# Kernel optimization log

Measured on AMD Instinct MI355X. Metric: run time of the kernel, lower is better.

The kernel has to match this reference:

```python
import jax, jax.numpy as jnp
import numpy as np

EPS = 1e-8  # torch.cosine_similarity default eps


def _gelu(x):
    # torch nn.GELU default = exact (erf) gelu
    return jax.nn.gelu(x, approximate=False)


def setup_inputs() -> dict:
    key = jax.random.key(0)
    ks = jax.random.split(key, 12)
    B, D, H1, E, N, K = 32768, 768, 256, 128, 500, 5
    TOT = D + E + 1 + 1 + 4  # 902, importance_net input dim
    s = 0.02
    return {
        "cue": jax.random.normal(ks[0], (B, D), jnp.float32),
        "internal_state": jnp.zeros((B, E), jnp.float32),
        "reward": jax.random.uniform(ks[1], (B, 1), dtype=jnp.float32),
        "timestamp": jax.random.uniform(ks[2], (B, 1), dtype=jnp.float32),
        "emotional_state": jax.random.uniform(ks[3], (B, 4), dtype=jnp.float32),
        "centroids": jax.random.normal(ks[4], (N, E), jnp.float32),
        "enc_w1": jax.random.normal(ks[5], (D, H1), jnp.float32) * s,
        "enc_b1": jnp.zeros((H1,), jnp.float32),
        "enc_w2": jax.random.normal(ks[6], (H1, E), jnp.float32) * s,
        "enc_b2": jnp.zeros((E,), jnp.float32),
        "imp_w1": jax.random.normal(ks[7], (TOT, 64), jnp.float32) * s,
        "imp_b1": jnp.zeros((64,), jnp.float32),
        "imp_w2": jax.random.normal(ks[8], (64, 1), jnp.float32) * s,
        "imp_b2": jnp.zeros((1,), jnp.float32),
        "top_k": K,
    }


def reference(cue, internal_state, reward, timestamp, emotional_state, centroids,
              enc_w1, enc_b1, enc_w2, enc_b2,
              imp_w1, imp_b1, imp_w2, imp_b2, top_k):
    # --- encoder MLP (batched over all cues instead of per-item calls) ---
    enc = _gelu(cue @ enc_w1 + enc_b1) @ enc_w2 + enc_b2        # [B, 128]

    # --- cosine similarity vs all cluster centroids (fused loop) ---
    num = enc @ centroids.T                                      # [B, N]
    e_n = jnp.linalg.norm(enc, axis=-1, keepdims=True)           # [B, 1]
    c_n = jnp.linalg.norm(centroids, axis=-1)                    # [N]
    sims = num / jnp.maximum(e_n * c_n[None, :], EPS)            # [B, N]
    top_vals, _ = jax.lax.top_k(sims, top_k)                     # [B, K]

    # --- importance net on combined memory entry ---
    combined = jnp.concatenate(
        [cue, internal_state, reward, timestamp, emotional_state], axis=-1)  # [B, 902]
    imp = jax.nn.sigmoid(_gelu(combined @ imp_w1 + imp_b1) @ imp_w2 + imp_b2)  # [B, 1]
    imp = imp * jnp.mean(emotional_state, axis=-1, keepdims=True)

    return jnp.concatenate([top_vals, imp], axis=-1)             # [B, K+1]
```

## Files before the change

kernel.cpp:

```cpp
#include <hip/hip_runtime.h>
#include <hip/hip_bf16.h>
#include <hip/hip_fp16.h>
#include <math.h>

using f32x4  = __attribute__((ext_vector_type(4))) float;
using half8  = __attribute__((ext_vector_type(8))) _Float16;
using uint4v = __attribute__((ext_vector_type(4))) unsigned int;

#define WAITV(N) asm volatile("s_waitcnt vmcnt(" #N ")" ::: "memory")
#define LGKM0    asm volatile("s_waitcnt lgkmcnt(0)" ::: "memory")

__device__ __forceinline__ unsigned short f32_to_f16u(float f) {
  return __half_as_ushort(__float2half(f));
}
__device__ __forceinline__ float f16u_to_f32(unsigned short h) {
  return __half2float(__ushort_as_half(h));
}
__device__ __forceinline__ unsigned int pk2(float a, float b) {
  return (unsigned int)f32_to_f16u(a) | ((unsigned int)f32_to_f16u(b) << 16);
}
__device__ __forceinline__ f32x4 mfma16(half8 a, half8 b, f32x4 c) {
  return __builtin_amdgcn_mfma_f32_16x16x32_f16(a, b, c, 0, 0, 0);
}
__device__ __forceinline__ void gload_lds16(void* lds, const void* g) {
  __builtin_amdgcn_global_load_lds(
      (const __attribute__((address_space(1))) unsigned int*)g,
      (__attribute__((address_space(3))) unsigned int*)lds, 16, 0, 0);
}
__device__ __forceinline__ float gelu_exact(float x) {
  return 0.5f * x * (1.0f + erff(x * 0.70710678118654752440f));
}


__global__ __launch_bounds__(256) void k_prep(
    const float* __restrict__ enc_w1, const float* __restrict__ enc_w2,
    const float* __restrict__ imp_w1, const float* __restrict__ cent,
    const float* __restrict__ reward, const float* __restrict__ tsp,
    const float* __restrict__ emo,
    unsigned short* __restrict__ W1T, unsigned short* __restrict__ W2T,
    unsigned short* __restrict__ impW1T, unsigned short* __restrict__ centC,
    float* __restrict__ c_n, unsigned short* __restrict__ tail) {
  int idx = blockIdx.x * 256 + threadIdx.x;
  if (idx < 256 * 768) {
    int n = idx / 768, k = idx - n * 768;
    W1T[idx] = f32_to_f16u(enc_w1[k * 256 + n]);
  }
  if (idx < 128 * 256) {
    int n = idx >> 8, k = idx & 255;
    W2T[idx] = f32_to_f16u(enc_w2[k * 128 + n]);
  }
  if (idx < 64 * 960) {
    int n = idx / 960, k = idx - n * 960;
    impW1T[idx] = (k < 902) ? f32_to_f16u(imp_w1[k * 64 + n]) : (unsigned short)0;
  }
  if (idx < 512 * 128) {
    int n = idx >> 7, k = idx & 127;
    centC[idx] = (n < 500) ? f32_to_f16u(cent[n * 128 + k]) : (unsigned short)0;
  }
  if (idx < 512) {
    float s = 0.f;
    if (idx < 500) {
      const f32x4* p = (const f32x4*)(cent + idx * 128);
#pragma unroll 8
      for (int j = 0; j < 32; ++j) {
        f32x4 v = p[j];
#pragma unroll
        for (int e = 0; e < 4; ++e) {
          float q = (float)(_Float16)v[e];
          s += q * q;
        }
      }
    }
    c_n[idx] = sqrtf(s);
  }
  if (idx < 32768) {
    f32x4 e4 = *(const f32x4*)(emo + (size_t)idx * 4);
    unsigned short* tp = tail + (size_t)idx * 8;
    tp[0] = f32_to_f16u(reward[idx]);
    tp[1] = f32_to_f16u(tsp[idx]);
    tp[2] = f32_to_f16u(e4[0]); tp[3] = f32_to_f16u(e4[1]);
    tp[4] = f32_to_f16u(e4[2]); tp[5] = f32_to_f16u(e4[3]);
    tp[6] = 0; tp[7] = 0;
  }
}

__global__ __launch_bounds__(512, 4) void k_encimp(
    const float* __restrict__ cue, const float* __restrict__ internal,
    const float* __restrict__ emo,
    const unsigned short* __restrict__ W1T, const unsigned short* __restrict__ impW1T,
    const unsigned short* __restrict__ tail,
    const float* __restrict__ b1, const float* __restrict__ ib1,
    const float* __restrict__ iw2, const float* __restrict__ ib2,
    unsigned short* __restrict__ h1, float* __restrict__ out) {
  __shared__ unsigned char sm[73728];
  const int t = threadIdx.x;
  const int lane = t & 63, w = t >> 6;
  const int wr = w >> 2, wc = w & 3;
  const int g = lane >> 4, c = lane & 15;
  const int row0 = blockIdx.x * 64;

  const int srow = t >> 3, q8 = t & 7;
  const int abyte = srow * 128 + q8 * 16;
  const int aswz = (srow & 7) << 4;
  const int myrow = row0 + srow;

  f32x4 aLo, aHi;
  auto issueA = [&](int j) {
    const float* s = (j < 12)
        ? (cue + (size_t)myrow * 768 + j * 64 + q8 * 8)
        : (internal + (size_t)myrow * 128 + (j - 12) * 64 + q8 * 8);
    aLo = *(const f32x4*)s;
    aHi = *(const f32x4*)(s + 4);
  };
  auto convWrite = [&](int buf) {
    uint4v u = {pk2(aLo[0], aLo[1]), pk2(aLo[2], aLo[3]),
                pk2(aHi[0], aHi[1]), pk2(aHi[2], aHi[3])};
    *(uint4v*)(sm + buf * 8192 + (abyte ^ aswz)) = u;
  };
  auto issueB1 = [&](int j) {
#pragma unroll
    for (int i = 0; i < 4; ++i) {
      int L = i * 8192 + t * 16;
      int nl = L >> 7, x = L & 127;
      gload_lds16(sm + 24576 + i * 8192 + w * 1024,
                  (const unsigned char*)W1T + ((size_t)nl * 768 + j * 64) * 2 +
                      (x ^ ((nl & 7) << 4)));
    }
  };
  auto issueB2 = [&](int j, int buf) {
    int L = t * 16, nl = L >> 7, x = L & 127;
    gload_lds16(sm + 57344 + buf * 8192 + w * 1024,
                (const unsigned char*)impW1T + (size_t)nl * 1920 + j * 128 +
                    (x ^ ((nl & 7) << 4)));
  };

  f32x4 acc1[2][4];
  f32x4 acc2[2];
#pragma unroll
  for (int i = 0; i < 2; ++i) {
    acc2[i] = f32x4{0.f, 0.f, 0.f, 0.f};
#pragma unroll
    for (int j = 0; j < 4; ++j) acc1[i][j] = f32x4{0.f, 0.f, 0.f, 0.f};
  }

  auto mfma_step = [&](int abuf, int b2buf, bool enc) {
    const unsigned char* Ab  = sm + abuf * 8192;
    const unsigned char* Bb2 = sm + 57344 + b2buf * 8192;
#pragma unroll
    for (int ks = 0; ks < 2; ++ks) {
      half8 af[2];
#pragma unroll
      for (int mf = 0; mf < 2; ++mf) {
        int m = wr * 32 + mf * 16 + c;
        af[mf] = *(const half8*)(Ab + m * 128 + ((ks * 64 + g * 16) ^ ((m & 7) << 4)));
      }
      {
        int n2 = wc * 16 + c;
        half8 b2f = *(const half8*)(Bb2 + n2 * 128 + ((ks * 64 + g * 16) ^ ((n2 & 7) << 4)));
        acc2[0] = mfma16(af[0], b2f, acc2[0]);
        acc2[1] = mfma16(af[1], b2f, acc2[1]);
      }
      if (enc) {
#pragma unroll
        for (int nf = 0; nf < 4; ++nf) {
          int n = wc * 64 + nf * 16 + c;
          half8 bf = *(const half8*)(sm + 24576 + n * 128 +
                                     ((ks * 64 + g * 16) ^ ((n & 7) << 4)));
          acc1[0][nf] = mfma16(af[0], bf, acc1[0][nf]);
          acc1[1][nf] = mfma16(af[1], bf, acc1[1][nf]);
        }
      }
    }
  };

  {
    uint4v tl = {0u, 0u, 0u, 0u};
    if (q8 == 0) tl = *(const uint4v*)(tail + (size_t)myrow * 8);
    issueA(0); issueB1(0); issueB2(0, 0);
    *(uint4v*)(sm + 16384 + (abyte ^ aswz)) = tl;
    convWrite(0);
    issueA(1); issueB2(1, 1);
    WAITV(3);
    LGKM0;
    __builtin_amdgcn_s_barrier();
  }

  int p = 0;
  for (int it = 0; it < 12; ++it) {
    mfma_step(p, p, true);
    convWrite(p ^ 1);
    LGKM0;
    __builtin_amdgcn_s_barrier();
    if (it < 11) issueB1(it + 1);
    issueA(it + 2);
    issueB2(it + 2, p);
    WAITV(3);
    __builtin_amdgcn_s_barrier();
    p ^= 1;
  }
  mfma_step(0, 0, false);
  convWrite(1);
  LGKM0;
  __builtin_amdgcn_s_barrier();
  issueB2(14, 0);
  WAITV(1);
  __builtin_amdgcn_s_barrier();
  mfma_step(1, 1, false);
  LGKM0;
  __builtin_amdgcn_s_barrier();
  WAITV(0);
  __builtin_amdgcn_s_barrier();
  mfma_step(2, 0, false);

  float bias1[4];
#pragma unroll
  for (int nf = 0; nf < 4; ++nf) bias1[nf] = b1[wc * 64 + nf * 16 + c];
#pragma unroll
  for (int mf = 0; mf < 2; ++mf)
#pragma unroll
    for (int nf = 0; nf < 4; ++nf)
#pragma unroll
      for (int rr = 0; rr < 4; ++rr) {
        float x = acc1[mf][nf][rr] + bias1[nf];
        int m = row0 + wr * 32 + mf * 16 + g * 4 + rr;
        int n = wc * 64 + nf * 16 + c;
        h1[(size_t)m * 256 + n] = f32_to_f16u(gelu_exact(x));
      }

  {
    float* s_p = (float*)(sm + 24576);
    float b1v = ib1[wc * 16 + c];
    float w2v = iw2[wc * 16 + c];
#pragma unroll
    for (int mf = 0; mf < 2; ++mf)
#pragma unroll
      for (int rr = 0; rr < 4; ++rr) {
        float v = gelu_exact(acc2[mf][rr] + b1v) * w2v;
        v += __shfl_xor(v, 1);
        v += __shfl_xor(v, 2);
        v += __shfl_xor(v, 4);
        v += __shfl_xor(v, 8);
        if (c == 0) s_p[(wr * 32 + mf * 16 + g * 4 + rr) * 4 + wc] = v;
      }
    __syncthreads();
    if (t < 64) {
      float ssum = s_p[t * 4 + 0] + s_p[t * 4 + 1] + s_p[t * 4 + 2] + s_p[t * 4 + 3];
      int rowA = row0 + t;
      float z = ssum + ib2[0];
      float sig = 1.0f / (1.0f + expf(-z));
      f32x4 e4 = *(const f32x4*)(emo + (size_t)rowA * 4);
      float m4 = 0.25f * (e4[0] + e4[1] + e4[2] + e4[3]);
      out[(size_t)rowA * 6 + 5] = sig * m4;
    }
  }
}

__global__ __launch_bounds__(256) void k_enc2(
    const unsigned short* __restrict__ h1, const unsigned short* __restrict__ W2T,
    const float* __restrict__ b2, unsigned short* __restrict__ enc) {
  __shared__ unsigned char smA[16384];
  __shared__ unsigned char smB[8192];
  const int t = threadIdx.x;
  const int lane = t & 63, w = t >> 6;
  const int wr = w >> 1, wc = w & 1;
  const int g = lane >> 4, c = lane & 15;
  const int row0 = blockIdx.x * 128;
  const int n0 = blockIdx.y * 64;

  f32x4 acc[4][2];
#pragma unroll
  for (int i = 0; i < 4; ++i)
#pragma unroll
    for (int j = 0; j < 2; ++j) acc[i][j] = f32x4{0.f, 0.f, 0.f, 0.f};

  for (int it = 0; it < 4; ++it) {
    __syncthreads();
#pragma unroll
    for (int i = 0; i < 4; ++i) {
      int L = i * 4096 + t * 16;
      int rl = L >> 7, x = L & 127;
      const unsigned char* gs = (const unsigned char*)h1 +
          (size_t)(row0 + rl) * 512 + it * 128 + (x ^ ((rl & 7) << 4));
      gload_lds16(smA + i * 4096 + w * 1024, gs);
    }
#pragma unroll
    for (int i = 0; i < 2; ++i) {
      int L = i * 4096 + t * 16;
      int nl = L >> 7, x = L & 127;
      const unsigned char* gs = (const unsigned char*)W2T +
          (size_t)(n0 + nl) * 512 + it * 128 + (x ^ ((nl & 7) << 4));
      gload_lds16(smB + i * 4096 + w * 1024, gs);
    }
    __syncthreads();
#pragma unroll
    for (int ks = 0; ks < 2; ++ks) {
      half8 af[4], bf[2];
#pragma unroll
      for (int mf = 0; mf < 4; ++mf) {
        int m = wr * 64 + mf * 16 + c;
        af[mf] = *(const half8*)(smA + m * 128 + (((ks * 64) + g * 16) ^ ((m & 7) << 4)));
      }
#pragma unroll
      for (int nf = 0; nf < 2; ++nf) {
        int n = wc * 32 + nf * 16 + c;
        bf[nf] = *(const half8*)(smB + n * 128 + (((ks * 64) + g * 16) ^ ((n & 7) << 4)));
      }
#pragma unroll
      for (int mf = 0; mf < 4; ++mf)
#pragma unroll
        for (int nf = 0; nf < 2; ++nf)
          acc[mf][nf] = mfma16(af[mf], bf[nf], acc[mf][nf]);
    }
  }
  float bias[2];
#pragma unroll
  for (int nf = 0; nf < 2; ++nf) bias[nf] = b2[n0 + wc * 32 + nf * 16 + c];
#pragma unroll
  for (int mf = 0; mf < 4; ++mf)
#pragma unroll
    for (int nf = 0; nf < 2; ++nf)
#pragma unroll
      for (int r = 0; r < 4; ++r) {
        float x = acc[mf][nf][r] + bias[nf];
        int m = row0 + wr * 64 + mf * 16 + g * 4 + r;
        int n = n0 + wc * 32 + nf * 16 + c;
        enc[(size_t)m * 128 + n] = f32_to_f16u(x);
      }
}

__global__ __launch_bounds__(256) void k_sims(
    const unsigned short* __restrict__ enc, const unsigned short* __restrict__ centC,
    const float* __restrict__ c_n, float* __restrict__ out) {
  __shared__ unsigned char smC[32768];
  __shared__ float s_en[64];
  const int t = threadIdx.x, lane = t & 63, w = t >> 6;
  const int g = lane >> 4, c = lane & 15;
  const int row0 = blockIdx.x * 64;

  {
    int r = t >> 2, q = t & 3;
    const unsigned char* base = (const unsigned char*)enc + (size_t)(row0 + r) * 256 + q * 64;
    float s = 0.f;
#pragma unroll
    for (int j = 0; j < 4; ++j) {
      uint4v u = *(const uint4v*)(base + j * 16);
#pragma unroll
      for (int e = 0; e < 4; ++e) {
        float lo = f16u_to_f32((unsigned short)(u[e] & 0xFFFFu));
        float hi = f16u_to_f32((unsigned short)(u[e] >> 16));
        s += lo * lo + hi * hi;
      }
    }
    s += __shfl_xor(s, 1);
    s += __shfl_xor(s, 2);
    if (q == 0) s_en[r] = sqrtf(s);
  }
  __syncthreads();

  float en[4];
#pragma unroll
  for (int r = 0; r < 4; ++r) en[r] = s_en[w * 16 + g * 4 + r];

  half8 af[4];
  {
    const unsigned char* abase =
        (const unsigned char*)enc + (size_t)(row0 + w * 16 + c) * 256 + g * 16;
#pragma unroll
    for (int kk = 0; kk < 4; ++kk) af[kk] = *(const half8*)(abase + kk * 64);
  }

  unsigned int top5[4][5];
#pragma unroll
  for (int r = 0; r < 4; ++r)
#pragma unroll
    for (int s5 = 0; s5 < 5; ++s5) top5[r][s5] = 0u;

#pragma unroll
  for (int ch = 0; ch < 4; ++ch) {
    __syncthreads();
#pragma unroll
    for (int i = 0; i < 8; ++i) {
      int L = i * 4096 + t * 16;
      int nl = L >> 8, x = L & 255;
      const unsigned char* gs = (const unsigned char*)centC +
          (size_t)(ch * 128 + nl) * 256 + (x ^ ((nl & 7) << 4));
      gload_lds16(smC + i * 4096 + w * 1024, gs);
    }
    __syncthreads();

    f32x4 acc[8];
#pragma unroll
    for (int i = 0; i < 8; ++i) acc[i] = f32x4{0.f, 0.f, 0.f, 0.f};
#pragma unroll
    for (int nfc = 0; nfc < 8; ++nfc) {
      int nl = nfc * 16 + c;
      const unsigned char* bbase = smC + nl * 256;
      int swz = (nl & 7) << 4;
#pragma unroll
      for (int kk = 0; kk < 4; ++kk) {
        half8 bf = *(const half8*)(bbase + ((kk * 64 + g * 16) ^ swz));
        acc[nfc] = mfma16(af[kk], bf, acc[nfc]);
      }
    }

#pragma unroll
    for (int nfc = 0; nfc < 8; ++nfc) {
      int col = ch * 128 + nfc * 16 + c;
      float cnv = c_n[col];
#pragma unroll
      for (int r = 0; r < 4; ++r) {
        float denom = fmaxf(en[r] * cnv, 1e-8f);
        float v = acc[nfc][r] * __builtin_amdgcn_rcpf(denom);
        unsigned int u = __float_as_uint(v);
        u = (u & 0x80000000u) ? ~u : (u | 0x80000000u);
        unsigned int k = (col < 500) ? ((u & 0xFFFFFE00u) | (unsigned)col) : 0u;
        unsigned int t0 = top5[r][0], t1 = top5[r][1], t2 = top5[r][2],
                     t3 = top5[r][3], t4 = top5[r][4];
        top5[r][0] = (k > t0) ? k : t0;
        top5[r][1] = (k > t0) ? t0 : ((k > t1) ? k : t1);
        top5[r][2] = (k > t1) ? t1 : ((k > t2) ? k : t2);
        top5[r][3] = (k > t2) ? t2 : ((k > t3) ? k : t3);
        top5[r][4] = (k > t3) ? t3 : ((k > t4) ? k : t4);
      }
    }
  }

#pragma unroll
  for (int r = 0; r < 4; ++r) {
    int rowA = row0 + w * 16 + g * 4 + r;
    unsigned int h0 = top5[r][0], h1 = top5[r][1], h2 = top5[r][2],
                 h3 = top5[r][3], h4 = top5[r][4];
#pragma unroll
    for (int it5 = 0; it5 < 5; ++it5) {
      unsigned int best = h0;
#pragma unroll
      for (int s = 1; s < 16; s <<= 1) {
        unsigned int o = __shfl_xor(best, s);
        best = (o > best) ? o : best;
      }
      if (c == 0) {
        unsigned int m = best & 0xFFFFFE00u;
        unsigned int uu = (m & 0x80000000u) ? (m ^ 0x80000000u) : ~m;
        out[(size_t)rowA * 6 + it5] = __uint_as_float(uu);
      }
      bool pop = (h0 == best);
      h0 = pop ? h1 : h0;
      h1 = pop ? h2 : h1;
      h2 = pop ? h3 : h2;
      h3 = pop ? h4 : h3;
      h4 = pop ? 0u : h4;
    }
  }
}

extern "C" void kernel_launch(void* const* d_in, const int* in_sizes, int n_in,
                              void* d_out, int out_size, void* d_ws, size_t ws_size,
                              hipStream_t stream) {
  (void)in_sizes; (void)n_in; (void)out_size; (void)ws_size;
  const float* cue      = (const float*)d_in[0];
  const float* internal = (const float*)d_in[1];
  const float* reward   = (const float*)d_in[2];
  const float* tsp      = (const float*)d_in[3];
  const float* emo      = (const float*)d_in[4];
  const float* cent     = (const float*)d_in[5];
  const float* enc_w1   = (const float*)d_in[6];
  const float* enc_b1   = (const float*)d_in[7];
  const float* enc_w2   = (const float*)d_in[8];
  const float* enc_b2   = (const float*)d_in[9];
  const float* imp_w1   = (const float*)d_in[10];
  const float* imp_b1   = (const float*)d_in[11];
  const float* imp_w2   = (const float*)d_in[12];
  const float* imp_b2   = (const float*)d_in[13];
  float* out = (float*)d_out;

  unsigned char* ws = (unsigned char*)d_ws;
  unsigned short* h1     = (unsigned short*)(ws + 0);
  unsigned short* enc    = (unsigned short*)(ws + 16777216);
  unsigned short* W1T    = (unsigned short*)(ws + 25165824);
  unsigned short* W2T    = (unsigned short*)(ws + 25559040);
  unsigned short* impW1T = (unsigned short*)(ws + 25624576);
  unsigned short* centC  = (unsigned short*)(ws + 25747456);
  float*          c_n    = (float*)(ws + 25878528);
  unsigned short* tail   = (unsigned short*)(ws + 25880576);

  k_prep<<<768, 256, 0, stream>>>(enc_w1, enc_w2, imp_w1, cent, reward, tsp, emo,
                                  W1T, W2T, impW1T, centC, c_n, tail);
  k_encimp<<<512, 512, 0, stream>>>(cue, internal, emo, W1T, impW1T, tail,
                                    enc_b1, imp_b1, imp_w2, imp_b2, h1, out);
  k_enc2<<<dim3(256, 2), 256, 0, stream>>>(h1, W2T, enc_b2, enc);
  k_sims<<<512, 256, 0, stream>>>(enc, centC, c_n, out);
}
```

Before: 74.37 us.

## Tile W1 transpose through LDS and overlap MFMA with next-stage loads

The prep kernel now transposes enc_w1 in 64x64 tiles staged through shared memory, so both the global reads and the writes are coalesced instead of strided. The main loop is restructured: B fragments are read into registers before the barrier, then the next-stage conversion write and global loads are issued before the MFMA block, which runs at raised wave priority. The aim is to overlap memory issue with matrix math and cut pipeline stalls. This adds register pressure and an extra LDS wait, and it changes the barrier ordering, so buffer-reuse correctness relies on the fragment reads completing first.

```diff
diff --git a/kernel.cpp b/kernel.cpp
--- a/kernel.cpp
+++ b/kernel.cpp
@@ -40,11 +40,27 @@
     unsigned short* __restrict__ W1T, unsigned short* __restrict__ W2T,
     unsigned short* __restrict__ impW1T, unsigned short* __restrict__ centC,
     float* __restrict__ c_n, unsigned short* __restrict__ tail) {
-  int idx = blockIdx.x * 256 + threadIdx.x;
-  if (idx < 256 * 768) {
-    int n = idx / 768, k = idx - n * 768;
-    W1T[idx] = f32_to_f16u(enc_w1[k * 256 + n]);
-  }
+  __shared__ float ld[64][65];
+  const int bx = blockIdx.x, t = threadIdx.x;
+  if (bx < 48) {
+    int tk = bx % 12, tn = bx / 12;
+    int k0 = tk * 64, n0 = tn * 64;
+    int cn = t & 63, r4 = t >> 6;
+#pragma unroll
+    for (int pass = 0; pass < 16; ++pass) {
+      int kk = pass * 4 + r4;
+      ld[kk][cn] = enc_w1[(size_t)(k0 + kk) * 256 + n0 + cn];
+    }
+    __syncthreads();
+    int ck = t & 63, rn4 = t >> 6;
+#pragma unroll
+    for (int pass = 0; pass < 16; ++pass) {
+      int nn = pass * 4 + rn4;
+      W1T[(size_t)(n0 + nn) * 768 + k0 + ck] = f32_to_f16u(ld[ck][nn]);
+    }
+    return;
+  }
+  int idx = (bx - 48) * 256 + t;
   if (idx < 128 * 256) {
     int n = idx >> 8, k = idx & 255;
     W2T[idx] = f32_to_f16u(enc_w2[k * 128 + n]);
@@ -187,14 +203,46 @@
 
   int p = 0;
   for (int it = 0; it < 12; ++it) {
-    mfma_step(p, p, true);
-    convWrite(p ^ 1);
+    half8 bf[2][4], b2f[2];
+#pragma unroll
+    for (int ks = 0; ks < 2; ++ks) {
+#pragma unroll
+      for (int nf = 0; nf < 4; ++nf) {
+        int n = wc * 64 + nf * 16 + c;
+        bf[ks][nf] = *(const half8*)(sm + 24576 + n * 128 +
+                                     ((ks * 64 + g * 16) ^ ((n & 7) << 4)));
+      }
+      int n2 = wc * 16 + c;
+      b2f[ks] = *(const half8*)(sm + 57344 + p * 8192 + n2 * 128 +
+                                ((ks * 64 + g * 16) ^ ((n2 & 7) << 4)));
+    }
     LGKM0;
     __builtin_amdgcn_s_barrier();
     if (it < 11) issueB1(it + 1);
+    convWrite(p ^ 1);
     issueA(it + 2);
     issueB2(it + 2, p);
+    __builtin_amdgcn_s_setprio(1);
+#pragma unroll
+    for (int ks = 0; ks < 2; ++ks) {
+      half8 af[2];
+#pragma unroll
+      for (int mf = 0; mf < 2; ++mf) {
+        int m = wr * 32 + mf * 16 + c;
+        af[mf] = *(const half8*)(sm + p * 8192 + m * 128 +
+                                 ((ks * 64 + g * 16) ^ ((m & 7) << 4)));
+      }
+      acc2[0] = mfma16(af[0], b2f[ks], acc2[0]);
+      acc2[1] = mfma16(af[1], b2f[ks], acc2[1]);
+#pragma unroll
+      for (int nf = 0; nf < 4; ++nf) {
+        acc1[0][nf] = mfma16(af[0], bf[ks][nf], acc1[0][nf]);
+        acc1[1][nf] = mfma16(af[1], bf[ks][nf], acc1[1][nf]);
+      }
+    }
+    __builtin_amdgcn_s_setprio(0);
     WAITV(3);
+    LGKM0;
     __builtin_amdgcn_s_barrier();
     p ^= 1;
   }
```

Result: slower. 75.92 us (+2.1%).

## Pre-tile weights k-group-major and warp-specialize loads in encoder/importance GEMM

Applied to the files above, without the earlier changes.

The prep kernel now writes W1 and the importance weights in a k-group-major tiled layout, with W1 transposed through an LDS tile. That lets the main kernel fill LDS with plain contiguous global-to-LDS copies and read MFMA fragments without XOR swizzling. The main GEMM loop moves from 64-wide to 32-wide K steps with smaller double buffers, cutting LDS use from 72 KB to 48 KB and raising the launch-bounds occupancy hint. Warps 0-3 load and convert the activation tile while warps 4-7 fetch the importance weights. In exchange the loop runs roughly twice as many iterations and barriers, and the higher occupancy may not help with only 512 blocks.

```diff
diff --git a/kernel.cpp b/kernel.cpp
--- a/kernel.cpp
+++ b/kernel.cpp
@@ -37,21 +37,39 @@
     const float* __restrict__ imp_w1, const float* __restrict__ cent,
     const float* __restrict__ reward, const float* __restrict__ tsp,
     const float* __restrict__ emo,
-    unsigned short* __restrict__ W1T, unsigned short* __restrict__ W2T,
-    unsigned short* __restrict__ impW1T, unsigned short* __restrict__ centC,
+    unsigned short* __restrict__ W1Tg, unsigned short* __restrict__ W2T,
+    unsigned short* __restrict__ impW1Tg, unsigned short* __restrict__ centC,
     float* __restrict__ c_n, unsigned short* __restrict__ tail) {
-  int idx = blockIdx.x * 256 + threadIdx.x;
-  if (idx < 256 * 768) {
-    int n = idx / 768, k = idx - n * 768;
-    W1T[idx] = f32_to_f16u(enc_w1[k * 256 + n]);
-  }
+  __shared__ float ld[64][65];
+  const int bx = blockIdx.x, t = threadIdx.x;
+  if (bx < 48) {
+    int tk = bx % 12, tn = bx / 12;
+    int k0 = tk * 64, n0 = tn * 64;
+    int cn = t & 63, r4 = t >> 6;
+#pragma unroll
+    for (int pass = 0; pass < 16; ++pass) {
+      int kk = pass * 4 + r4;
+      ld[kk][cn] = enc_w1[(size_t)(k0 + kk) * 256 + n0 + cn];
+    }
+    __syncthreads();
+    int ck = t & 63, rn4 = t >> 6;
+#pragma unroll
+    for (int pass = 0; pass < 16; ++pass) {
+      int nn = pass * 4 + rn4;
+      int k = k0 + ck, n = n0 + nn;
+      W1Tg[(size_t)(k >> 3) * 2048 + n * 8 + (k & 7)] = f32_to_f16u(ld[ck][nn]);
+    }
+    return;
+  }
+  int idx = (bx - 48) * 256 + t;
   if (idx < 128 * 256) {
     int n = idx >> 8, k = idx & 255;
     W2T[idx] = f32_to_f16u(enc_w2[k * 128 + n]);
   }
   if (idx < 64 * 960) {
     int n = idx / 960, k = idx - n * 960;
-    impW1T[idx] = (k < 902) ? f32_to_f16u(imp_w1[k * 64 + n]) : (unsigned short)0;
+    unsigned short v = (k < 902) ? f32_to_f16u(imp_w1[k * 64 + n]) : (unsigned short)0;
+    impW1Tg[(size_t)(k >> 3) * 512 + n * 8 + (k & 7)] = v;
   }
   if (idx < 512 * 128) {
     int n = idx >> 7, k = idx & 127;
@@ -84,54 +102,63 @@
   }
 }
 
-__global__ __launch_bounds__(512, 4) void k_encimp(
+__global__ __launch_bounds__(512, 6) void k_encimp(
     const float* __restrict__ cue, const float* __restrict__ internal,
     const float* __restrict__ emo,
-    const unsigned short* __restrict__ W1T, const unsigned short* __restrict__ impW1T,
+    const unsigned short* __restrict__ W1Tg, const unsigned short* __restrict__ impW1Tg,
     const unsigned short* __restrict__ tail,
     const float* __restrict__ b1, const float* __restrict__ ib1,
     const float* __restrict__ iw2, const float* __restrict__ ib2,
     unsigned short* __restrict__ h1, float* __restrict__ out) {
-  __shared__ unsigned char sm[73728];
+  __shared__ unsigned char sm[49152];
   const int t = threadIdx.x;
   const int lane = t & 63, w = t >> 6;
   const int wr = w >> 2, wc = w & 3;
   const int g = lane >> 4, c = lane & 15;
   const int row0 = blockIdx.x * 64;
-
-  const int srow = t >> 3, q8 = t & 7;
-  const int abyte = srow * 128 + q8 * 16;
-  const int aswz = (srow & 7) << 4;
-  const int myrow = row0 + srow;
+  const bool isA = (w < 4);
+
+  const int arow = t >> 2, aq = t & 3;
+  const int amrow = row0 + arow;
 
   f32x4 aLo, aHi;
-  auto issueA = [&](int j) {
-    const float* s = (j < 12)
-        ? (cue + (size_t)myrow * 768 + j * 64 + q8 * 8)
-        : (internal + (size_t)myrow * 128 + (j - 12) * 64 + q8 * 8);
-    aLo = *(const f32x4*)s;
-    aHi = *(const f32x4*)(s + 4);
+  uint4v tailv;
+  auto loadA = [&](int jj) {
+    if (jj < 24) {
+      const float* s = cue + (size_t)amrow * 768 + jj * 32 + aq * 8;
+      aLo = *(const f32x4*)s; aHi = *(const f32x4*)(s + 4);
+    } else if (jj < 28) {
+      const float* s = internal + (size_t)amrow * 128 + (jj - 24) * 32 + aq * 8;
+      aLo = *(const f32x4*)s; aHi = *(const f32x4*)(s + 4);
+    } else {
+      if (aq == 0) tailv = *(const uint4v*)(tail + (size_t)amrow * 8);
+    }
   };
-  auto convWrite = [&](int buf) {
-    uint4v u = {pk2(aLo[0], aLo[1]), pk2(aLo[2], aLo[3]),
-                pk2(aHi[0], aHi[1]), pk2(aHi[2], aHi[3])};
-    *(uint4v*)(sm + buf * 8192 + (abyte ^ aswz)) = u;
+  auto convW = [&](int jj, int buf) {
+    uint4v u;
+    if (jj < 28) {
+      u = uint4v{pk2(aLo[0], aLo[1]), pk2(aLo[2], aLo[3]),
+                 pk2(aHi[0], aHi[1]), pk2(aHi[2], aHi[3])};
+    } else {
+      u = (aq == 0) ? tailv : uint4v{0u, 0u, 0u, 0u};
+    }
+    *(uint4v*)(sm + buf * 4096 + aq * 1024 + arow * 16) = u;
   };
-  auto issueB1 = [&](int j) {
-#pragma unroll
-    for (int i = 0; i < 4; ++i) {
-      int L = i * 8192 + t * 16;
-      int nl = L >> 7, x = L & 127;
-      gload_lds16(sm + 24576 + i * 8192 + w * 1024,
-                  (const unsigned char*)W1T + ((size_t)nl * 768 + j * 64) * 2 +
-                      (x ^ ((nl & 7) << 4)));
+  auto issueB1 = [&](int jj) {
+#pragma unroll
+    for (int i = 0; i < 2; ++i) {
+      int q = w * 2 + i;
+      int gg = q >> 2, nq = q & 3;
+      gload_lds16(sm + 8192 + (jj & 1) * 16384 + gg * 4096 + nq * 1024,
+                  (const unsigned char*)W1Tg +
+                      ((size_t)(jj * 4 + gg) * 256 + nq * 64 + lane) * 16);
     }
   };
-  auto issueB2 = [&](int j, int buf) {
-    int L = t * 16, nl = L >> 7, x = L & 127;
-    gload_lds16(sm + 57344 + buf * 8192 + w * 1024,
-                (const unsigned char*)impW1T + (size_t)nl * 1920 + j * 128 +
-                    (x ^ ((nl & 7) << 4)));
+  auto issueB2 = [&](int jj, int buf) {
+    int gg = w & 3;
+    gload_lds16(sm + 40960 + buf * 4096 + gg * 1024,
+                (const unsigned char*)impW1Tg +
+                    ((size_t)(jj * 4 + gg) * 64 + lane) * 16);
   };
 
   f32x4 acc1[2][4];
@@ -143,74 +170,73 @@
     for (int j = 0; j < 4; ++j) acc1[i][j] = f32x4{0.f, 0.f, 0.f, 0.f};
   }
 
-  auto mfma_step = [&](int abuf, int b2buf, bool enc) {
-    const unsigned char* Ab  = sm + abuf * 8192;
-    const unsigned char* Bb2 = sm + 57344 + b2buf * 8192;
-#pragma unroll
-    for (int ks = 0; ks < 2; ++ks) {
-      half8 af[2];
-#pragma unroll
-      for (int mf = 0; mf < 2; ++mf) {
-        int m = wr * 32 + mf * 16 + c;
-        af[mf] = *(const half8*)(Ab + m * 128 + ((ks * 64 + g * 16) ^ ((m & 7) << 4)));
-      }
-      {
-        int n2 = wc * 16 + c;
-        half8 b2f = *(const half8*)(Bb2 + n2 * 128 + ((ks * 64 + g * 16) ^ ((n2 & 7) << 4)));
-        acc2[0] = mfma16(af[0], b2f, acc2[0]);
-        acc2[1] = mfma16(af[1], b2f, acc2[1]);
-      }
-      if (enc) {
-#pragma unroll
-        for (int nf = 0; nf < 4; ++nf) {
-          int n = wc * 64 + nf * 16 + c;
-          half8 bf = *(const half8*)(sm + 24576 + n * 128 +
-                                     ((ks * 64 + g * 16) ^ ((n & 7) << 4)));
-          acc1[0][nf] = mfma16(af[0], bf, acc1[0][nf]);
-          acc1[1][nf] = mfma16(af[1], bf, acc1[1][nf]);
-        }
-      }
+  auto mfma_full = [&](int ab, int b2b) {
+    const unsigned char* A = sm + ab * 4096;
+    half8 af0 = *(const half8*)(A + g * 1024 + (wr * 32 + c) * 16);
+    half8 af1 = *(const half8*)(A + g * 1024 + (wr * 32 + 16 + c) * 16);
+    {
+      half8 b2f = *(const half8*)(sm + 40960 + b2b * 4096 + g * 1024 + (wc * 16 + c) * 16);
+      acc2[0] = mfma16(af0, b2f, acc2[0]);
+      acc2[1] = mfma16(af1, b2f, acc2[1]);
+    }
+    const unsigned char* B1 = sm + 8192 + (ab) * 16384;
+#pragma unroll
+    for (int nf = 0; nf < 4; ++nf) {
+      half8 bf = *(const half8*)(B1 + g * 4096 + (wc * 64 + nf * 16 + c) * 16);
+      acc1[0][nf] = mfma16(af0, bf, acc1[0][nf]);
+      acc1[1][nf] = mfma16(af1, bf, acc1[1][nf]);
     }
   };
-
-  {
-    uint4v tl = {0u, 0u, 0u, 0u};
-    if (q8 == 0) tl = *(const uint4v*)(tail + (size_t)myrow * 8);
-    issueA(0); issueB1(0); issueB2(0, 0);
-    *(uint4v*)(sm + 16384 + (abyte ^ aswz)) = tl;
-    convWrite(0);
-    issueA(1); issueB2(1, 1);
+  auto mfma_imp = [&](int ab, int b2b) {
+    const unsigned char* A = sm + ab * 4096;
+    half8 af0 = *(const half8*)(A + g * 1024 + (wr * 32 + c) * 16);
+    half8 af1 = *(const half8*)(A + g * 1024 + (wr * 32 + 16 + c) * 16);
+    half8 b2f = *(const half8*)(sm + 40960 + b2b * 4096 + g * 1024 + (wc * 16 + c) * 16);
+    acc2[0] = mfma16(af0, b2f, acc2[0]);
+    acc2[1] = mfma16(af1, b2f, acc2[1]);
+  };
+
+  if (isA) {
+    loadA(0);
+    issueB1(0);
+    convW(0, 0);
+    issueB1(1);
+    loadA(1);
+  } else {
+    issueB2(0, 0);
+    issueB1(0);
+    issueB2(1, 1);
+    issueB1(1);
     WAITV(3);
+  }
+  LGKM0;
+  __builtin_amdgcn_s_barrier();
+
+  for (int j = 0; j < 22; ++j) {
+    mfma_full(j & 1, j & 1);
+    if (isA) convW(j + 1, (j + 1) & 1);
     LGKM0;
     __builtin_amdgcn_s_barrier();
-  }
-
-  int p = 0;
-  for (int it = 0; it < 12; ++it) {
-    mfma_step(p, p, true);
-    convWrite(p ^ 1);
+    issueB1(j + 2);
+    if (isA) loadA(j + 2);
+    else     issueB2(j + 2, j & 1);
+    if (!isA) { WAITV(3); }
+    __builtin_amdgcn_s_barrier();
+  }
+  for (int j = 22; j < 28; ++j) {
+    if (j < 24) mfma_full(j & 1, j & 1);
+    else        mfma_imp(j & 1, j & 1);
+    if (isA) convW(j + 1, (j + 1) & 1);
     LGKM0;
     __builtin_amdgcn_s_barrier();
-    if (it < 11) issueB1(it + 1);
-    issueA(it + 2);
-    issueB2(it + 2, p);
-    WAITV(3);
+    if (j + 2 <= 28) {
+      if (isA) loadA(j + 2);
+      else     issueB2(j + 2, j & 1);
+    }
+    WAITV(0);
     __builtin_amdgcn_s_barrier();
-    p ^= 1;
-  }
-  mfma_step(0, 0, false);
-  convWrite(1);
-  LGKM0;
-  __builtin_amdgcn_s_barrier();
-  issueB2(14, 0);
-  WAITV(1);
-  __builtin_amdgcn_s_barrier();
-  mfma_step(1, 1, false);
-  LGKM0;
-  __builtin_amdgcn_s_barrier();
-  WAITV(0);
-  __builtin_amdgcn_s_barrier();
-  mfma_step(2, 0, false);
+  }
+  mfma_imp(0, 0);
 
   float bias1[4];
 #pragma unroll
@@ -228,7 +254,7 @@
       }
 
   {
-    float* s_p = (float*)(sm + 24576);
+    float* s_p = (float*)(sm + 8192);
     float b1v = ib1[wc * 16 + c];
     float w2v = iw2[wc * 16 + c];
 #pragma unroll
@@ -476,16 +502,16 @@
   unsigned char* ws = (unsigned char*)d_ws;
   unsigned short* h1     = (unsigned short*)(ws + 0);
   unsigned short* enc    = (unsigned short*)(ws + 16777216);
-  unsigned short* W1T    = (unsigned short*)(ws + 25165824);
+  unsigned short* W1Tg   = (unsigned short*)(ws + 25165824);
   unsigned short* W2T    = (unsigned short*)(ws + 25559040);
-  unsigned short* impW1T = (unsigned short*)(ws + 25624576);
+  unsigned short* impW1Tg= (unsigned short*)(ws + 25624576);
   unsigned short* centC  = (unsigned short*)(ws + 25747456);
   float*          c_n    = (float*)(ws + 25878528);
   unsigned short* tail   = (unsigned short*)(ws + 25880576);
 
   k_prep<<<768, 256, 0, stream>>>(enc_w1, enc_w2, imp_w1, cent, reward, tsp, emo,
-                                  W1T, W2T, impW1T, centC, c_n, tail);
-  k_encimp<<<512, 512, 0, stream>>>(cue, internal, emo, W1T, impW1T, tail,
+                                  W1Tg, W2T, impW1Tg, centC, c_n, tail);
+  k_encimp<<<512, 512, 0, stream>>>(cue, internal, emo, W1Tg, impW1Tg, tail,
                                     enc_b1, imp_b1, imp_w2, imp_b2, h1, out);
   k_enc2<<<dim3(256, 2), 256, 0, stream>>>(h1, W2T, enc_b2, enc);
   k_sims<<<512, 256, 0, stream>>>(enc, centC, c_n, out);
```

Result: slower. 87.13 us (+17.2%).

## Fuse encoder second layer into similarity top-k kernel; tile W1 transpose through LDS

Applied to the files above, without the earlier changes.

The second encoder GEMM moves into the cosine-similarity/top-k kernel, so one launch now produces the encoded rows and their norms. Row norms are taken from the fp16-rounded accumulator values instead of re-reading the encoded rows. The encoded rows are still written to global memory and read back by the same block, but that read should mostly hit cache. The prep kernel's W1 transpose now goes through a 64x64 LDS tile so both its reads and writes are coalesced, which lets the prep grid shrink. In exchange, the fused kernel uses more shared memory per block, and its global write-then-read ordering within a block relies on a vmcnt wait plus a barrier.

```diff
diff --git a/kernel.cpp b/kernel.cpp
--- a/kernel.cpp
+++ b/kernel.cpp
@@ -40,11 +40,27 @@
     unsigned short* __restrict__ W1T, unsigned short* __restrict__ W2T,
     unsigned short* __restrict__ impW1T, unsigned short* __restrict__ centC,
     float* __restrict__ c_n, unsigned short* __restrict__ tail) {
-  int idx = blockIdx.x * 256 + threadIdx.x;
-  if (idx < 256 * 768) {
-    int n = idx / 768, k = idx - n * 768;
-    W1T[idx] = f32_to_f16u(enc_w1[k * 256 + n]);
-  }
+  __shared__ float ld[64][65];
+  const int bx = blockIdx.x, t = threadIdx.x;
+  if (bx < 48) {
+    int tk = bx % 12, tn = bx / 12;
+    int k0 = tk * 64, n0 = tn * 64;
+    int cn = t & 63, r4 = t >> 6;
+#pragma unroll
+    for (int pass = 0; pass < 16; ++pass) {
+      int kk = pass * 4 + r4;
+      ld[kk][cn] = enc_w1[(size_t)(k0 + kk) * 256 + n0 + cn];
+    }
+    __syncthreads();
+    int ck = t & 63, rn4 = t >> 6;
+#pragma unroll
+    for (int pass = 0; pass < 16; ++pass) {
+      int nn = pass * 4 + rn4;
+      W1T[(size_t)(n0 + nn) * 768 + k0 + ck] = f32_to_f16u(ld[ck][nn]);
+    }
+    return;
+  }
+  int idx = (bx - 48) * 256 + t;
   if (idx < 128 * 256) {
     int n = idx >> 8, k = idx & 255;
     W2T[idx] = f32_to_f16u(enc_w2[k * 128 + n]);
@@ -255,118 +271,106 @@
   }
 }
 
-__global__ __launch_bounds__(256) void k_enc2(
+__global__ __launch_bounds__(256) void k_tail(
     const unsigned short* __restrict__ h1, const unsigned short* __restrict__ W2T,
-    const float* __restrict__ b2, unsigned short* __restrict__ enc) {
-  __shared__ unsigned char smA[16384];
-  __shared__ unsigned char smB[8192];
-  const int t = threadIdx.x;
-  const int lane = t & 63, w = t >> 6;
-  const int wr = w >> 1, wc = w & 1;
-  const int g = lane >> 4, c = lane & 15;
-  const int row0 = blockIdx.x * 128;
-  const int n0 = blockIdx.y * 64;
-
-  f32x4 acc[4][2];
-#pragma unroll
-  for (int i = 0; i < 4; ++i)
-#pragma unroll
-    for (int j = 0; j < 2; ++j) acc[i][j] = f32x4{0.f, 0.f, 0.f, 0.f};
-
-  for (int it = 0; it < 4; ++it) {
-    __syncthreads();
-#pragma unroll
-    for (int i = 0; i < 4; ++i) {
-      int L = i * 4096 + t * 16;
-      int rl = L >> 7, x = L & 127;
-      const unsigned char* gs = (const unsigned char*)h1 +
-          (size_t)(row0 + rl) * 512 + it * 128 + (x ^ ((rl & 7) << 4));
-      gload_lds16(smA + i * 4096 + w * 1024, gs);
-    }
-#pragma unroll
-    for (int i = 0; i < 2; ++i) {
-      int L = i * 4096 + t * 16;
-      int nl = L >> 7, x = L & 127;
-      const unsigned char* gs = (const unsigned char*)W2T +
-          (size_t)(n0 + nl) * 512 + it * 128 + (x ^ ((nl & 7) << 4));
-      gload_lds16(smB + i * 4096 + w * 1024, gs);
-    }
-    __syncthreads();
-#pragma unroll
-    for (int ks = 0; ks < 2; ++ks) {
-      half8 af[4], bf[2];
-#pragma unroll
-      for (int mf = 0; mf < 4; ++mf) {
-        int m = wr * 64 + mf * 16 + c;
-        af[mf] = *(const half8*)(smA + m * 128 + (((ks * 64) + g * 16) ^ ((m & 7) << 4)));
-      }
-#pragma unroll
-      for (int nf = 0; nf < 2; ++nf) {
-        int n = wc * 32 + nf * 16 + c;
-        bf[nf] = *(const half8*)(smB + n * 128 + (((ks * 64) + g * 16) ^ ((n & 7) << 4)));
-      }
-#pragma unroll
-      for (int mf = 0; mf < 4; ++mf)
-#pragma unroll
-        for (int nf = 0; nf < 2; ++nf)
-          acc[mf][nf] = mfma16(af[mf], bf[nf], acc[mf][nf]);
-    }
-  }
-  float bias[2];
-#pragma unroll
-  for (int nf = 0; nf < 2; ++nf) bias[nf] = b2[n0 + wc * 32 + nf * 16 + c];
-#pragma unroll
-  for (int mf = 0; mf < 4; ++mf)
-#pragma unroll
-    for (int nf = 0; nf < 2; ++nf)
-#pragma unroll
-      for (int r = 0; r < 4; ++r) {
-        float x = acc[mf][nf][r] + bias[nf];
-        int m = row0 + wr * 64 + mf * 16 + g * 4 + r;
-        int n = n0 + wc * 32 + nf * 16 + c;
-        enc[(size_t)m * 128 + n] = f32_to_f16u(x);
-      }
-}
-
-__global__ __launch_bounds__(256) void k_sims(
-    const unsigned short* __restrict__ enc, const unsigned short* __restrict__ centC,
-    const float* __restrict__ c_n, float* __restrict__ out) {
-  __shared__ unsigned char smC[32768];
+    const unsigned short* __restrict__ centC, const float* __restrict__ c_n,
+    const float* __restrict__ b2, unsigned short* __restrict__ enc,
+    float* __restrict__ out) {
+  __shared__ unsigned char smA[32768];
+  __shared__ unsigned char smB[32768];
+  __shared__ float s_pn[256];
   __shared__ float s_en[64];
   const int t = threadIdx.x, lane = t & 63, w = t >> 6;
   const int g = lane >> 4, c = lane & 15;
   const int row0 = blockIdx.x * 64;
 
-  {
-    int r = t >> 2, q = t & 3;
-    const unsigned char* base = (const unsigned char*)enc + (size_t)(row0 + r) * 256 + q * 64;
-    float s = 0.f;
-#pragma unroll
-    for (int j = 0; j < 4; ++j) {
-      uint4v u = *(const uint4v*)(base + j * 16);
-#pragma unroll
-      for (int e = 0; e < 4; ++e) {
-        float lo = f16u_to_f32((unsigned short)(u[e] & 0xFFFFu));
-        float hi = f16u_to_f32((unsigned short)(u[e] >> 16));
-        s += lo * lo + hi * hi;
-      }
-    }
-    s += __shfl_xor(s, 1);
-    s += __shfl_xor(s, 2);
-    if (q == 0) s_en[r] = sqrtf(s);
-  }
+#pragma unroll
+  for (int i = 0; i < 8; ++i) {
+    int L = i * 4096 + t * 16;
+    int rl = L >> 9, x = L & 511;
+    gload_lds16(smA + i * 4096 + w * 1024,
+                (const unsigned char*)h1 + (size_t)(row0 + rl) * 512 +
+                    (x ^ ((rl & 7) << 4)));
+  }
+
+  float nsq[4][4];
+#pragma unroll
+  for (int mf = 0; mf < 4; ++mf)
+#pragma unroll
+    for (int rr = 0; rr < 4; ++rr) nsq[mf][rr] = 0.f;
+
+  for (int h = 0; h < 2; ++h) {
+#pragma unroll
+    for (int i = 0; i < 8; ++i) {
+      int L = i * 4096 + t * 16;
+      int nl = L >> 9, x = L & 511;
+      gload_lds16(smB + i * 4096 + w * 1024,
+                  (const unsigned char*)W2T + (size_t)(h * 64 + nl) * 512 +
+                      (x ^ ((nl & 7) << 4)));
+    }
+    __syncthreads();
+
+    f32x4 acc_e[4];
+#pragma unroll
+    for (int mf = 0; mf < 4; ++mf) acc_e[mf] = f32x4{0.f, 0.f, 0.f, 0.f};
+#pragma unroll
+    for (int ks = 0; ks < 8; ++ks) {
+      half8 af[4];
+#pragma unroll
+      for (int mf = 0; mf < 4; ++mf) {
+        int rl = mf * 16 + c;
+        af[mf] = *(const half8*)(smA + rl * 512 +
+                                 ((ks * 64 + g * 16) ^ ((rl & 7) << 4)));
+      }
+      int nl = w * 16 + c;
+      half8 bf = *(const half8*)(smB + nl * 512 +
+                                 ((ks * 64 + g * 16) ^ ((nl & 7) << 4)));
+#pragma unroll
+      for (int mf = 0; mf < 4; ++mf) acc_e[mf] = mfma16(af[mf], bf, acc_e[mf]);
+    }
+    float bias = b2[h * 64 + w * 16 + c];
+#pragma unroll
+    for (int mf = 0; mf < 4; ++mf)
+#pragma unroll
+      for (int rr = 0; rr < 4; ++rr) {
+        float x = acc_e[mf][rr] + bias;
+        unsigned short hv = f32_to_f16u(x);
+        float xr = f16u_to_f32(hv);
+        nsq[mf][rr] += xr * xr;
+        int m = row0 + mf * 16 + g * 4 + rr;
+        enc[(size_t)m * 128 + h * 64 + w * 16 + c] = hv;
+      }
+    __syncthreads();
+  }
+
+#pragma unroll
+  for (int mf = 0; mf < 4; ++mf)
+#pragma unroll
+    for (int rr = 0; rr < 4; ++rr) {
+      float v = nsq[mf][rr];
+      v += __shfl_xor(v, 1);
+      v += __shfl_xor(v, 2);
+      v += __shfl_xor(v, 4);
+      v += __shfl_xor(v, 8);
+      if (c == 0) s_pn[(mf * 16 + g * 4 + rr) * 4 + w] = v;
+    }
+  WAITV(0);
   __syncthreads();
+  if (t < 64)
+    s_en[t] = sqrtf(s_pn[t * 4 + 0] + s_pn[t * 4 + 1] +
+                    s_pn[t * 4 + 2] + s_pn[t * 4 + 3]);
+  __syncthreads();
 
   float en[4];
 #pragma unroll
   for (int r = 0; r < 4; ++r) en[r] = s_en[w * 16 + g * 4 + r];
 
-  half8 af[4];
+  half8 af2[4];
   {
     const unsigned char* abase =
         (const unsigned char*)enc + (size_t)(row0 + w * 16 + c) * 256 + g * 16;
 #pragma unroll
-    for (int kk = 0; kk < 4; ++kk) af[kk] = *(const half8*)(abase + kk * 64);
+    for (int kk = 0; kk < 4; ++kk) af2[kk] = *(const half8*)(abase + kk * 64);
   }
 
   unsigned int top5[4][5];
@@ -384,7 +388,7 @@
       int nl = L >> 8, x = L & 255;
       const unsigned char* gs = (const unsigned char*)centC +
           (size_t)(ch * 128 + nl) * 256 + (x ^ ((nl & 7) << 4));
-      gload_lds16(smC + i * 4096 + w * 1024, gs);
+      gload_lds16(smB + i * 4096 + w * 1024, gs);
     }
     __syncthreads();
 
@@ -394,12 +398,12 @@
 #pragma unroll
     for (int nfc = 0; nfc < 8; ++nfc) {
       int nl = nfc * 16 + c;
-      const unsigned char* bbase = smC + nl * 256;
+      const unsigned char* bbase = smB + nl * 256;
       int swz = (nl & 7) << 4;
 #pragma unroll
       for (int kk = 0; kk < 4; ++kk) {
         half8 bf = *(const half8*)(bbase + ((kk * 64 + g * 16) ^ swz));
-        acc[nfc] = mfma16(af[kk], bf, acc[nfc]);
+        acc[nfc] = mfma16(af2[kk], bf, acc[nfc]);
       }
     }
 
@@ -428,7 +432,7 @@
 #pragma unroll
   for (int r = 0; r < 4; ++r) {
     int rowA = row0 + w * 16 + g * 4 + r;
-    unsigned int h0 = top5[r][0], h1 = top5[r][1], h2 = top5[r][2],
+    unsigned int h0 = top5[r][0], h1v = top5[r][1], h2 = top5[r][2],
                  h3 = top5[r][3], h4 = top5[r][4];
 #pragma unroll
     for (int it5 = 0; it5 < 5; ++it5) {
@@ -444,8 +448,8 @@
         out[(size_t)rowA * 6 + it5] = __uint_as_float(uu);
       }
       bool pop = (h0 == best);
-      h0 = pop ? h1 : h0;
-      h1 = pop ? h2 : h1;
+      h0 = pop ? h1v : h0;
+      h1v = pop ? h2 : h1v;
       h2 = pop ? h3 : h2;
       h3 = pop ? h4 : h3;
       h4 = pop ? 0u : h4;
@@ -483,10 +487,9 @@
   float*          c_n    = (float*)(ws + 25878528);
   unsigned short* tail   = (unsigned short*)(ws + 25880576);
 
-  k_prep<<<768, 256, 0, stream>>>(enc_w1, enc_w2, imp_w1, cent, reward, tsp, emo,
+  k_prep<<<304, 256, 0, stream>>>(enc_w1, enc_w2, imp_w1, cent, reward, tsp, emo,
                                   W1T, W2T, impW1T, centC, c_n, tail);
   k_encimp<<<512, 512, 0, stream>>>(cue, internal, emo, W1T, impW1T, tail,
                                     enc_b1, imp_b1, imp_w2, imp_b2, h1, out);
-  k_enc2<<<dim3(256, 2), 256, 0, stream>>>(h1, W2T, enc_b2, enc);
-  k_sims<<<512, 256, 0, stream>>>(enc, centC, c_n, out);
-}
+  k_tail<<<512, 256, 0, stream>>>(h1, W2T, centC, c_n, enc_b2, enc, out);
+}
```

New measurement: 72.19 us. 2.9% less time.
